# Kernel tuning notes

Measured on AMD Instinct MI355X. Metric: run time of the kernel, lower is better.

The kernel has to match this reference:

```python
import jax, jax.numpy as jnp
from jax import lax
import numpy as np

N_FEAT = 256
ALPHA = 0.95
MIN_UNIT_NORM = 0.001
MAX_UNIT_NORM = 0.0001


def setup_inputs() -> dict:
    key = jax.random.key(0)
    spec = jax.random.normal(key, (16, 1, 257, 8000), dtype=jnp.float32)  # [B, C=1, F, T]
    # buffer from init_unit_norm_state: linspace(min, max, n_feat)
    unit_norm_state = jnp.linspace(MIN_UNIT_NORM, MAX_UNIT_NORM, N_FEAT, dtype=jnp.float32)
    return {"spec": spec, "unit_norm_state": unit_norm_state}


def reference(spec, unit_norm_state):
    # squeeze channel dim, keep first n_feat frequency bands -> [B, n_feat, T]
    x = spec[:, 0, :N_FEAT, :]
    B = x.shape[0]
    # running EMA norm state, broadcast to per-batch lanes: [B, n_feat]
    s0 = jnp.broadcast_to(unit_norm_state, (B, N_FEAT))
    xt = jnp.moveaxis(x, -1, 0)  # [T, B, n_feat] for scan over time

    def step(s, x_t):
        s = jnp.abs(x_t) * (1.0 - ALPHA) + s * ALPHA
        return s, x_t / jnp.sqrt(s)

    _, y = lax.scan(step, s0, xt)  # y: [T, B, n_feat]
    return jnp.moveaxis(y, 0, -1)[:, None]  # [B, 1, n_feat, T]
```

## Files before the change

kernel.cpp:

```cpp
#include <hip/hip_runtime.h>
#include <math.h>


#define ALPHA   0.95f
#define OMA     0.05f
#define TLEN    8000
#define CHUNK   16
#define NACT    500

#define A16_1   0.44012666865f
#define A16_2   0.19371148547f
#define A16_4   0.03752413897f
#define A16_8   0.00140806094f
#define A16_16  1.98263565e-06f
#define A16_32  3.93084413e-12f
#define A1024   1.54515294e-23f
#define LOG2_A16 (-1.18400927f)

__global__ __launch_bounds__(512) void fse_kernel(
    const float* __restrict__ spec,
    const float* __restrict__ uns,
    float* __restrict__ out)
{
    const int bf = blockIdx.x;
    const int b  = bf >> 8;
    const int f  = bf & 255;
    const float* inrow  = spec + ((size_t)b * 257 + (size_t)f) * TLEN;
    float*       outrow = out  + ((size_t)bf) * TLEN;

    const int tid  = threadIdx.x;
    const int lane = tid & 63;
    const int w    = tid >> 6;
    const bool active = (tid < NACT);

    float4 xq[4];
    float d = 0.0f;
    if (active) {
        const float4* p = (const float4*)(inrow + tid * CHUNK);
#pragma unroll
        for (int i = 0; i < 4; ++i) xq[i] = p[i];
#pragma unroll
        for (int i = 0; i < 4; ++i) {
            d = fmaf(fabsf(xq[i].x), OMA, d * ALPHA);
            d = fmaf(fabsf(xq[i].y), OMA, d * ALPHA);
            d = fmaf(fabsf(xq[i].z), OMA, d * ALPHA);
            d = fmaf(fabsf(xq[i].w), OMA, d * ALPHA);
        }
    }

    float v = d, t;
    t = __shfl_up(v, 1);  if (lane >= 1)  v = fmaf(A16_1,  t, v);
    t = __shfl_up(v, 2);  if (lane >= 2)  v = fmaf(A16_2,  t, v);
    t = __shfl_up(v, 4);  if (lane >= 4)  v = fmaf(A16_4,  t, v);
    t = __shfl_up(v, 8);  if (lane >= 8)  v = fmaf(A16_8,  t, v);
    t = __shfl_up(v, 16); if (lane >= 16) v = fmaf(A16_16, t, v);
    t = __shfl_up(v, 32); if (lane >= 32) v = fmaf(A16_32, t, v);

    __shared__ float tot[8];
    if (lane == 63) tot[w] = v;
    __syncthreads();
    float carry = 0.0f;
    for (int j = 0; j < w; ++j) carry = fmaf(carry, A1024, tot[j]);

    float e = __shfl_up(v, 1);
    if (lane == 0) e = 0.0f;
    e = fmaf(exp2f(LOG2_A16 * (float)lane), carry, e);

    const float s0 = uns[f];
    float s = fmaf(exp2f(LOG2_A16 * (float)tid), s0, e);

    if (active) {
#pragma unroll
        for (int i = 0; i < 4; ++i) {
            s = fmaf(fabsf(xq[i].x), OMA, s * ALPHA); xq[i].x = xq[i].x * rsqrtf(s);
            s = fmaf(fabsf(xq[i].y), OMA, s * ALPHA); xq[i].y = xq[i].y * rsqrtf(s);
            s = fmaf(fabsf(xq[i].z), OMA, s * ALPHA); xq[i].z = xq[i].z * rsqrtf(s);
            s = fmaf(fabsf(xq[i].w), OMA, s * ALPHA); xq[i].w = xq[i].w * rsqrtf(s);
        }
        float4* q = (float4*)(outrow + tid * CHUNK);
#pragma unroll
        for (int i = 0; i < 4; ++i) q[i] = xq[i];
    }
}

extern "C" void kernel_launch(void* const* d_in, const int* in_sizes, int n_in,
                              void* d_out, int out_size, void* d_ws, size_t ws_size,
                              hipStream_t stream) {
    const float* spec = (const float*)d_in[0];
    const float* uns  = (const float*)d_in[1];
    float* out = (float*)d_out;
    (void)in_sizes; (void)n_in; (void)d_ws; (void)ws_size; (void)out_size;

    dim3 grid(16 * 256);
    dim3 block(512);
    fse_kernel<<<grid, block, 0, stream>>>(spec, uns, out);
}
```

Before: 236.8 us.

## Split row into four segments for coalesced float4 loads and stores

Changes the per-thread data layout so each thread owns one float4 in each of four contiguous 2000-element segments, instead of a 16-element contiguous chunk. Warp loads and stores become fully coalesced. The scan is run on the four segments in parallel, and segment boundary states are stitched through shared memory. This adds a second block barrier and extra shuffle and scan work per thread, in exchange for better global memory access patterns.

New measurement: 230.2 us. 2.8% less time.

```diff
diff --git a/kernel.cpp b/kernel.cpp
--- a/kernel.cpp
+++ b/kernel.cpp
@@ -2,20 +2,20 @@
 #include <math.h>
 
 
-#define ALPHA   0.95f
-#define OMA     0.05f
-#define TLEN    8000
-#define CHUNK   16
-#define NACT    500
+#define TLEN   8000
+#define SEGLEN 2000
+#define NCHUNK 500
+#define ALPHA  0.95f
+#define OMA    0.05f
 
-#define A16_1   0.44012666865f
-#define A16_2   0.19371148547f
-#define A16_4   0.03752413897f
-#define A16_8   0.00140806094f
-#define A16_16  1.98263565e-06f
-#define A16_32  3.93084413e-12f
-#define A1024   1.54515294e-23f
-#define LOG2_A16 (-1.18400927f)
+#define A4_1   0.81450625f
+#define A4_2   0.66342043f
+#define A4_4   0.44012667f
+#define A4_8   0.19371149f
+#define A4_16  0.03752414f
+#define A4_32  0.00140806f
+#define A256   1.98263565e-06f
+#define LOG2_A4 (-0.29600231f)
 
 __global__ __launch_bounds__(512) void fse_kernel(
     const float* __restrict__ spec,
@@ -31,55 +31,90 @@
     const int tid  = threadIdx.x;
     const int lane = tid & 63;
     const int w    = tid >> 6;
-    const bool active = (tid < NACT);
+    const bool active = (tid < NCHUNK);
 
     float4 xq[4];
-    float d = 0.0f;
-    if (active) {
-        const float4* p = (const float4*)(inrow + tid * CHUNK);
 #pragma unroll
-        for (int i = 0; i < 4; ++i) xq[i] = p[i];
-#pragma unroll
-        for (int i = 0; i < 4; ++i) {
-            d = fmaf(fabsf(xq[i].x), OMA, d * ALPHA);
-            d = fmaf(fabsf(xq[i].y), OMA, d * ALPHA);
-            d = fmaf(fabsf(xq[i].z), OMA, d * ALPHA);
-            d = fmaf(fabsf(xq[i].w), OMA, d * ALPHA);
-        }
+    for (int k = 0; k < 4; ++k) {
+        if (active)
+            xq[k] = *(const float4*)(inrow + k * SEGLEN + tid * 4);
     }
 
-    float v = d, t;
-    t = __shfl_up(v, 1);  if (lane >= 1)  v = fmaf(A16_1,  t, v);
-    t = __shfl_up(v, 2);  if (lane >= 2)  v = fmaf(A16_2,  t, v);
-    t = __shfl_up(v, 4);  if (lane >= 4)  v = fmaf(A16_4,  t, v);
-    t = __shfl_up(v, 8);  if (lane >= 8)  v = fmaf(A16_8,  t, v);
-    t = __shfl_up(v, 16); if (lane >= 16) v = fmaf(A16_16, t, v);
-    t = __shfl_up(v, 32); if (lane >= 32) v = fmaf(A16_32, t, v);
+    float v[4];
+#pragma unroll
+    for (int k = 0; k < 4; ++k) {
+        float d = 0.0f;
+        if (active) {
+            d = fmaf(fabsf(xq[k].x), OMA, d * ALPHA);
+            d = fmaf(fabsf(xq[k].y), OMA, d * ALPHA);
+            d = fmaf(fabsf(xq[k].z), OMA, d * ALPHA);
+            d = fmaf(fabsf(xq[k].w), OMA, d * ALPHA);
+        }
+        v[k] = d;
+    }
 
-    __shared__ float tot[8];
-    if (lane == 63) tot[w] = v;
+#define SCAN_STEP(D, C)                                                \
+    {                                                                  \
+        float t0 = __shfl_up(v[0], D);                                 \
+        float t1 = __shfl_up(v[1], D);                                 \
+        float t2 = __shfl_up(v[2], D);                                 \
+        float t3 = __shfl_up(v[3], D);                                 \
+        if (lane >= D) {                                               \
+            v[0] = fmaf(C, t0, v[0]);                                  \
+            v[1] = fmaf(C, t1, v[1]);                                  \
+            v[2] = fmaf(C, t2, v[2]);                                  \
+            v[3] = fmaf(C, t3, v[3]);                                  \
+        }                                                              \
+    }
+    SCAN_STEP(1,  A4_1)
+    SCAN_STEP(2,  A4_2)
+    SCAN_STEP(4,  A4_4)
+    SCAN_STEP(8,  A4_8)
+    SCAN_STEP(16, A4_16)
+    SCAN_STEP(32, A4_32)
+#undef SCAN_STEP
+
+    __shared__ float tot[4][8];
+    __shared__ float segend[4];
+    if (lane == 63) {
+#pragma unroll
+        for (int k = 0; k < 4; ++k) tot[k][w] = v[k];
+    }
     __syncthreads();
-    float carry = 0.0f;
-    for (int j = 0; j < w; ++j) carry = fmaf(carry, A1024, tot[j]);
 
-    float e = __shfl_up(v, 1);
-    if (lane == 0) e = 0.0f;
-    e = fmaf(exp2f(LOG2_A16 * (float)lane), carry, e);
+    const float pl = exp2f(LOG2_A4 * (float)lane);
+    float e[4];
+#pragma unroll
+    for (int k = 0; k < 4; ++k) {
+        float carry = 0.0f;
+        for (int j = 0; j < w; ++j) carry = fmaf(carry, A256, tot[k][j]);
+        float ex = __shfl_up(v[k], 1);
+        if (lane == 0) ex = 0.0f;
+        e[k] = fmaf(pl, carry, ex);
+        if (tid == NCHUNK - 1 && k < 3)
+            segend[k] = fmaf(pl * A4_1, carry, v[k]);
+    }
+    __syncthreads();
 
+    const float pt = exp2f(LOG2_A4 * (float)tid);
     const float s0 = uns[f];
-    float s = fmaf(exp2f(LOG2_A16 * (float)tid), s0, e);
+    float S0[4];
+    S0[0] = s0;
+    S0[1] = segend[0];
+    S0[2] = segend[1];
+    S0[3] = segend[2];
 
-    if (active) {
 #pragma unroll
-        for (int i = 0; i < 4; ++i) {
-            s = fmaf(fabsf(xq[i].x), OMA, s * ALPHA); xq[i].x = xq[i].x * rsqrtf(s);
-            s = fmaf(fabsf(xq[i].y), OMA, s * ALPHA); xq[i].y = xq[i].y * rsqrtf(s);
-            s = fmaf(fabsf(xq[i].z), OMA, s * ALPHA); xq[i].z = xq[i].z * rsqrtf(s);
-            s = fmaf(fabsf(xq[i].w), OMA, s * ALPHA); xq[i].w = xq[i].w * rsqrtf(s);
+    for (int k = 0; k < 4; ++k) {
+        if (active) {
+            float s = fmaf(pt, S0[k], e[k]);
+            float4 r = xq[k];
+            s = fmaf(fabsf(r.x), OMA, s * ALPHA); r.x = r.x * rsqrtf(s);
+            s = fmaf(fabsf(r.y), OMA, s * ALPHA); r.y = r.y * rsqrtf(s);
+            s = fmaf(fabsf(r.z), OMA, s * ALPHA); r.z = r.z * rsqrtf(s);
+            s = fmaf(fabsf(r.w), OMA, s * ALPHA); r.w = r.w * rsqrtf(s);
+            *(float4*)(outrow + k * SEGLEN + tid * 4) = r;
         }
-        float4* q = (float4*)(outrow + tid * CHUNK);
-#pragma unroll
-        for (int i = 0; i < 4; ++i) q[i] = xq[i];
     }
 }
 
```

## Process each row with one wavefront looping over chunks with carried EMA state

Applied to the files above, without the earlier changes.

Each row is now handled by a single 64-lane wavefront instead of a 512-thread block. The wavefront walks the row in 31 float4 chunks, doing a wave-level scan per chunk and carrying the EMA state between chunks, with a two-deep register prefetch of the next chunks and a separate scalar tail. This removes the shared-memory barrier and the idle threads of the old layout, and the per-chunk loads become coalesced. In exchange each wave runs a serial chain of 31 scans, so latency hiding depends on occupancy and the prefetch.

After: 241.5 us. No clear change (+2.0%).

```diff
diff --git a/kernel.cpp b/kernel.cpp
--- a/kernel.cpp
+++ b/kernel.cpp
@@ -2,84 +2,104 @@
 #include <math.h>
 
 
+#define TLEN    8000
+#define NITER   31
+#define TAILOFF 7936
 #define ALPHA   0.95f
 #define OMA     0.05f
-#define TLEN    8000
-#define CHUNK   16
-#define NACT    500
 
-#define A16_1   0.44012666865f
-#define A16_2   0.19371148547f
-#define A16_4   0.03752413897f
-#define A16_8   0.00140806094f
-#define A16_16  1.98263565e-06f
-#define A16_32  3.93084413e-12f
-#define A1024   1.54515294e-23f
-#define LOG2_A16 (-1.18400927f)
+#define A4_1   0.81450625f
+#define A4_2   0.66342043f
+#define A4_4   0.44012667f
+#define A4_8   0.19371149f
+#define A4_16  0.03752414f
+#define A4_32  0.00140806f
+#define A256   1.98263565e-06f
+#define A1_1   0.95f
+#define A1_2   0.9025f
+#define A1_4   0.81450625f
+#define A1_8   0.66342043f
+#define A1_16  0.44012667f
+#define A1_32  0.19371149f
+#define LOG2_A1 (-0.07400058f)
+#define LOG2_A4 (-0.29600231f)
 
-__global__ __launch_bounds__(512) void fse_kernel(
+__global__ __launch_bounds__(256) void fse_kernel(
     const float* __restrict__ spec,
     const float* __restrict__ uns,
     float* __restrict__ out)
 {
-    const int bf = blockIdx.x;
-    const int b  = bf >> 8;
-    const int f  = bf & 255;
-    const float* inrow  = spec + ((size_t)b * 257 + (size_t)f) * TLEN;
-    float*       outrow = out  + ((size_t)bf) * TLEN;
-
     const int tid  = threadIdx.x;
     const int lane = tid & 63;
-    const int w    = tid >> 6;
-    const bool active = (tid < NACT);
+    const int wv   = tid >> 6;
+    const int bf   = blockIdx.x * 4 + wv;
+    const int b    = bf >> 8;
+    const int f    = bf & 255;
 
-    float4 xq[4];
-    float d = 0.0f;
-    if (active) {
-        const float4* p = (const float4*)(inrow + tid * CHUNK);
-#pragma unroll
-        for (int i = 0; i < 4; ++i) xq[i] = p[i];
-#pragma unroll
-        for (int i = 0; i < 4; ++i) {
-            d = fmaf(fabsf(xq[i].x), OMA, d * ALPHA);
-            d = fmaf(fabsf(xq[i].y), OMA, d * ALPHA);
-            d = fmaf(fabsf(xq[i].z), OMA, d * ALPHA);
-            d = fmaf(fabsf(xq[i].w), OMA, d * ALPHA);
+    const float*  inrow  = spec + ((size_t)b * 257 + (size_t)f) * TLEN;
+    float*        outrow = out  + ((size_t)bf) * TLEN;
+    const float4* pin  = (const float4*)inrow;
+    float4*       pout = (float4*)outrow;
+
+    const float pl4 = exp2f(LOG2_A4 * (float)lane);
+    float carry = uns[f];
+
+    float4 P0 = pin[lane];
+    float4 P1 = pin[64 + lane];
+
+#pragma unroll 2
+    for (int i = 0; i < NITER; ++i) {
+        float4 x = (i & 1) ? P1 : P0;
+        if (i + 2 < NITER) {
+            float4 nf = pin[(i + 2) * 64 + lane];
+            if (i & 1) P1 = nf; else P0 = nf;
         }
+
+        float d;
+        d = OMA * fabsf(x.x);
+        d = fmaf(fabsf(x.y), OMA, d * ALPHA);
+        d = fmaf(fabsf(x.z), OMA, d * ALPHA);
+        d = fmaf(fabsf(x.w), OMA, d * ALPHA);
+
+        float v = d, t;
+        t = __shfl_up(v, 1);  if (lane >= 1)  v = fmaf(A4_1,  t, v);
+        t = __shfl_up(v, 2);  if (lane >= 2)  v = fmaf(A4_2,  t, v);
+        t = __shfl_up(v, 4);  if (lane >= 4)  v = fmaf(A4_4,  t, v);
+        t = __shfl_up(v, 8);  if (lane >= 8)  v = fmaf(A4_8,  t, v);
+        t = __shfl_up(v, 16); if (lane >= 16) v = fmaf(A4_16, t, v);
+        t = __shfl_up(v, 32); if (lane >= 32) v = fmaf(A4_32, t, v);
+
+        float e = __shfl_up(v, 1);
+        if (lane == 0) e = 0.0f;
+        float s = fmaf(pl4, carry, e);
+
+        float incl63 = __shfl(v, 63);
+        carry = fmaf(A256, carry, incl63);
+
+        s = fmaf(fabsf(x.x), OMA, s * ALPHA); x.x *= rsqrtf(s);
+        s = fmaf(fabsf(x.y), OMA, s * ALPHA); x.y *= rsqrtf(s);
+        s = fmaf(fabsf(x.z), OMA, s * ALPHA); x.z *= rsqrtf(s);
+        s = fmaf(fabsf(x.w), OMA, s * ALPHA); x.w *= rsqrtf(s);
+
+        pout[i * 64 + lane] = x;
     }
 
-    float v = d, t;
-    t = __shfl_up(v, 1);  if (lane >= 1)  v = fmaf(A16_1,  t, v);
-    t = __shfl_up(v, 2);  if (lane >= 2)  v = fmaf(A16_2,  t, v);
-    t = __shfl_up(v, 4);  if (lane >= 4)  v = fmaf(A16_4,  t, v);
-    t = __shfl_up(v, 8);  if (lane >= 8)  v = fmaf(A16_8,  t, v);
-    t = __shfl_up(v, 16); if (lane >= 16) v = fmaf(A16_16, t, v);
-    t = __shfl_up(v, 32); if (lane >= 32) v = fmaf(A16_32, t, v);
+    {
+        float xt = inrow[TAILOFF + lane];
+        float v = OMA * fabsf(xt), t;
+        t = __shfl_up(v, 1);  if (lane >= 1)  v = fmaf(A1_1,  t, v);
+        t = __shfl_up(v, 2);  if (lane >= 2)  v = fmaf(A1_2,  t, v);
+        t = __shfl_up(v, 4);  if (lane >= 4)  v = fmaf(A1_4,  t, v);
+        t = __shfl_up(v, 8);  if (lane >= 8)  v = fmaf(A1_8,  t, v);
+        t = __shfl_up(v, 16); if (lane >= 16) v = fmaf(A1_16, t, v);
+        t = __shfl_up(v, 32); if (lane >= 32) v = fmaf(A1_32, t, v);
 
-    __shared__ float tot[8];
-    if (lane == 63) tot[w] = v;
-    __syncthreads();
-    float carry = 0.0f;
-    for (int j = 0; j < w; ++j) carry = fmaf(carry, A1024, tot[j]);
-
-    float e = __shfl_up(v, 1);
-    if (lane == 0) e = 0.0f;
-    e = fmaf(exp2f(LOG2_A16 * (float)lane), carry, e);
-
-    const float s0 = uns[f];
-    float s = fmaf(exp2f(LOG2_A16 * (float)tid), s0, e);
-
-    if (active) {
-#pragma unroll
-        for (int i = 0; i < 4; ++i) {
-            s = fmaf(fabsf(xq[i].x), OMA, s * ALPHA); xq[i].x = xq[i].x * rsqrtf(s);
-            s = fmaf(fabsf(xq[i].y), OMA, s * ALPHA); xq[i].y = xq[i].y * rsqrtf(s);
-            s = fmaf(fabsf(xq[i].z), OMA, s * ALPHA); xq[i].z = xq[i].z * rsqrtf(s);
-            s = fmaf(fabsf(xq[i].w), OMA, s * ALPHA); xq[i].w = xq[i].w * rsqrtf(s);
-        }
-        float4* q = (float4*)(outrow + tid * CHUNK);
-#pragma unroll
-        for (int i = 0; i < 4; ++i) q[i] = xq[i];
+        float e = __shfl_up(v, 1);
+        if (lane == 0) e = 0.0f;
+        const float pl1 = exp2f(LOG2_A1 * (float)lane);
+        float s = fmaf(pl1, carry, e);
+        s = fmaf(fabsf(xt), OMA, s * ALPHA);
+        outrow[TAILOFF + lane] = xt * rsqrtf(s);
     }
 }
 
@@ -91,7 +111,7 @@
     float* out = (float*)d_out;
     (void)in_sizes; (void)n_in; (void)d_ws; (void)ws_size; (void)out_size;
 
-    dim3 grid(16 * 256);
-    dim3 block(512);
+    dim3 grid(4096 / 4);
+    dim3 block(256);
     fse_kernel<<<grid, block, 0, stream>>>(spec, uns, out);
 }
```
